# Optimization experiments

Measured on AMD Instinct MI355X. Metric: run time of the kernel, lower is better.

## Reference

```python
import jax, jax.numpy as jnp
import numpy as np

T, B = 100, 512
DIMS = [700, 512, 20]
ALPHA = 0.8   # 1 - dt/tau_s = 1 - 0.001/0.005
BETA = 0.9    # 1 - dt/tau_m = 1 - 0.001/0.010
THR = 1.0     # snntorch default threshold


@jax.custom_vjp
def spike(x):
    # Heaviside with ATan surrogate gradient (snntorch default, alpha=2)
    return (x > 0).astype(x.dtype)

def _spike_fwd(x):
    return spike(x), x

def _spike_bwd(x, g):
    # d/dx atan surrogate with alpha=2: 1 / (1 + (pi*x)^2)
    return (g / (1.0 + (jnp.pi * x) ** 2),)

spike.defvjp(_spike_fwd, _spike_bwd)


def setup_inputs() -> dict:
    key = jax.random.key(0)
    kx, k1, k2 = jax.random.split(key, 3)
    x = jax.random.uniform(kx, (T, B, DIMS[0]), dtype=jnp.float32)
    # kaiming_normal_ on weight [d2, d1]: std = sqrt(2 / fan_in), fan_in = d1
    W1 = jax.random.normal(k1, (DIMS[1], DIMS[0]), dtype=jnp.float32) * np.sqrt(2.0 / DIMS[0])
    W2 = jax.random.normal(k2, (DIMS[2], DIMS[1]), dtype=jnp.float32) * np.sqrt(2.0 / DIMS[1])
    return {"x": x, "W1": W1, "W2": W2}


def _spiking_linear(x, W):
    # x: [T, B, d_in], W: [d_out, d_in]
    pre = jnp.einsum('tbi,oi->tbo', x, W)  # per-timestep F.linear, batched over T

    def step(carry, p):
        syn, mem = carry
        syn = ALPHA * syn + p
        # reset from previous-step membrane, detached (snntorch mem_reset)
        reset = jax.lax.stop_gradient((mem > THR).astype(p.dtype))
        mem = (BETA * mem + syn) * (1.0 - reset)  # reset_mechanism='zero'
        spk = spike(mem - THR)
        return (syn, mem), spk

    z = jnp.zeros(pre.shape[1:], dtype=pre.dtype)
    _, spks = jax.lax.scan(step, (z, z), pre)
    return spks  # [T, B, d_out]


def reference(x, W1, W2):
    x = x.astype(jnp.float32)
    s1 = _spiking_linear(x, W1)
    s2 = _spiking_linear(s1, W2)
    # SNN2.forward returns (out, all_spikes=[layer1_spikes, layer2_spikes])
    return (s2, s1, s2)
```

## Files before the change

kernel.cpp:

```cpp
#include <hip/hip_runtime.h>

#define T_STEPS 100
#define BATCH   512
#define D0      700
#define D1      512
#define D2      20
#define M_ROWS  (T_STEPS * BATCH)

#define OFF_S2A 0
#define OFF_S1  (T_STEPS * BATCH * D2)
#define OFF_S2B (OFF_S1 + T_STEPS * BATCH * D1)

__device__ __constant__ const float kALPHA = 0.8f;
__device__ __constant__ const float kBETA  = 0.9f;
__device__ __constant__ const float kTHR   = 1.0f;

constexpr int BM = 128, BN = 128, BK = 32;

__device__ __forceinline__ int swz(int k, int m) {
    const int c = m >> 2;
    const int cpos = c ^ ((c >> 3) & 3) ^ ((k >> 2) & 7);
    return k * BM + (cpos << 2) + (m & 3);
}

__global__ __launch_bounds__(256)
void gemm1_kernel(const float* __restrict__ A, const float* __restrict__ W,
                  float* __restrict__ C) {
    __shared__ float As[BK * BM];
    __shared__ float Ws[BK * BN];

    const int tid  = threadIdx.x;
    const int row0 = blockIdx.x * BM;
    const int col0 = blockIdx.y * BN;

    const int tx = tid & 15;
    const int ty = tid >> 4;

    const int ca0 = (2 * ty)     ^ (((2 * ty)     >> 3) & 3);
    const int ca1 = (2 * ty + 1) ^ (((2 * ty + 1) >> 3) & 3);
    const int cb0 = (2 * tx)     ^ (((2 * tx)     >> 3) & 3);
    const int cb1 = (2 * tx + 1) ^ (((2 * tx + 1) >> 3) & 3);

    float acc[8][8];
#pragma unroll
    for (int i = 0; i < 8; ++i)
#pragma unroll
        for (int j = 0; j < 8; ++j) acc[i][j] = 0.f;

    const int NT = (D0 + BK - 1) / BK;
    for (int kt = 0; kt < NT; ++kt) {
        const int k0 = kt * BK;
#pragma unroll
        for (int l = 0; l < 4; ++l) {
            const int f  = tid + l * 256;
            const int r  = f >> 3;
            const int c4 = f & 7;
            const int k  = c4 * 4;
            const int gk = k0 + k;

            float4 v, w;
            if (gk + 3 < D0) {
                v = *(const float4*)(A + (size_t)(row0 + r) * D0 + gk);
                w = *(const float4*)(W + (size_t)(col0 + r) * D0 + gk);
            } else {
                const float* ap = A + (size_t)(row0 + r) * D0;
                const float* wp = W + (size_t)(col0 + r) * D0;
                v.x = (gk + 0 < D0) ? ap[gk + 0] : 0.f;
                v.y = (gk + 1 < D0) ? ap[gk + 1] : 0.f;
                v.z = (gk + 2 < D0) ? ap[gk + 2] : 0.f;
                v.w = (gk + 3 < D0) ? ap[gk + 3] : 0.f;
                w.x = (gk + 0 < D0) ? wp[gk + 0] : 0.f;
                w.y = (gk + 1 < D0) ? wp[gk + 1] : 0.f;
                w.z = (gk + 2 < D0) ? wp[gk + 2] : 0.f;
                w.w = (gk + 3 < D0) ? wp[gk + 3] : 0.f;
            }
            As[swz(k + 0, r)] = v.x; As[swz(k + 1, r)] = v.y;
            As[swz(k + 2, r)] = v.z; As[swz(k + 3, r)] = v.w;
            Ws[swz(k + 0, r)] = w.x; Ws[swz(k + 1, r)] = w.y;
            Ws[swz(k + 2, r)] = w.z; Ws[swz(k + 3, r)] = w.w;
        }
        __syncthreads();

#pragma unroll
        for (int k = 0; k < BK; ++k) {
            const int kx = (k >> 2) & 7;
            const int kb = k * BM;
            float a[8], b[8];
            *(float4*)&a[0] = *(const float4*)&As[kb + ((ca0 ^ kx) << 2)];
            *(float4*)&a[4] = *(const float4*)&As[kb + ((ca1 ^ kx) << 2)];
            *(float4*)&b[0] = *(const float4*)&Ws[kb + ((cb0 ^ kx) << 2)];
            *(float4*)&b[4] = *(const float4*)&Ws[kb + ((cb1 ^ kx) << 2)];
#pragma unroll
            for (int i = 0; i < 8; ++i)
#pragma unroll
                for (int j = 0; j < 8; ++j)
                    acc[i][j] = fmaf(a[i], b[j], acc[i][j]);
        }
        __syncthreads();
    }

#pragma unroll
    for (int i = 0; i < 8; ++i) {
        float* cp = C + (size_t)(row0 + ty * 8 + i) * D1 + col0 + tx * 8;
        float4 v0 = make_float4(acc[i][0], acc[i][1], acc[i][2], acc[i][3]);
        float4 v1 = make_float4(acc[i][4], acc[i][5], acc[i][6], acc[i][7]);
        *(float4*)(cp + 0) = v0;
        *(float4*)(cp + 4) = v1;
    }
}

__global__ __launch_bounds__(256)
void scan1_kernel(float* __restrict__ buf) {
#pragma clang fp contract(off)
    const int idx = blockIdx.x * blockDim.x + threadIdx.x;
    const int stride = BATCH * D1;
    float syn = 0.f, mem = 0.f;
    float* p = buf + idx;
    for (int t = 0; t < T_STEPS; ++t) {
        const float pre = p[(size_t)t * stride];
        float a = kALPHA * syn;
        syn = a + pre;
        const float reset = (mem > kTHR) ? 1.f : 0.f;
        float bm = kBETA * mem;
        mem = (bm + syn) * (1.f - reset);
        p[(size_t)t * stride] = (mem > kTHR) ? 1.f : 0.f;
    }
}

__global__ __launch_bounds__(256)
void gemm2_kernel(const float* __restrict__ S1, const float* __restrict__ W2,
                  float* __restrict__ C) {
    __shared__ float Wsh[D2 * D1];
    for (int i = threadIdx.x; i < (D2 * D1) / 4; i += 256)
        ((float4*)Wsh)[i] = ((const float4*)W2)[i];
    __syncthreads();

    const int r  = threadIdx.x >> 2;
    const int kq = threadIdx.x & 3;
    const int m  = blockIdx.x * 64 + r;

    const float4* src = (const float4*)(S1 + (size_t)m * D1 + kq * 128);
    float acc[D2];
#pragma unroll
    for (int o = 0; o < D2; ++o) acc[o] = 0.f;

    for (int j = 0; j < 32; ++j) {
        const float4 v = src[j];
        const float* wbase = Wsh + kq * 128 + j * 4;
#pragma unroll
        for (int o = 0; o < D2; ++o) {
            const float4 w = *(const float4*)(wbase + o * D1);
            acc[o] += v.x * w.x + v.y * w.y + v.z * w.z + v.w * w.w;
        }
    }
#pragma unroll
    for (int o = 0; o < D2; ++o) {
        acc[o] += __shfl_xor(acc[o], 1);
        acc[o] += __shfl_xor(acc[o], 2);
    }
    if (kq == 0) {
        float* cp = C + (size_t)m * D2;
#pragma unroll
        for (int o = 0; o < D2; o += 4)
            *(float4*)(cp + o) = make_float4(acc[o], acc[o + 1], acc[o + 2], acc[o + 3]);
    }
}

__global__ __launch_bounds__(256)
void scan2_kernel(float* __restrict__ buf, float* __restrict__ dup) {
#pragma clang fp contract(off)
    const int idx = blockIdx.x * blockDim.x + threadIdx.x;
    const int stride = BATCH * D2;
    float syn = 0.f, mem = 0.f;
    for (int t = 0; t < T_STEPS; ++t) {
        const size_t off = (size_t)t * stride + idx;
        const float pre = buf[off];
        float a = kALPHA * syn;
        syn = a + pre;
        const float reset = (mem > kTHR) ? 1.f : 0.f;
        float bm = kBETA * mem;
        mem = (bm + syn) * (1.f - reset);
        const float s = (mem > kTHR) ? 1.f : 0.f;
        buf[off] = s;
        dup[off] = s;
    }
}

extern "C" void kernel_launch(void* const* d_in, const int* in_sizes, int n_in,
                              void* d_out, int out_size, void* d_ws, size_t ws_size,
                              hipStream_t stream) {
    const float* x  = (const float*)d_in[0];
    const float* W1 = (const float*)d_in[1];
    const float* W2 = (const float*)d_in[2];
    float* out = (float*)d_out;

    float* s2a = out + OFF_S2A;
    float* s1  = out + OFF_S1;
    float* s2b = out + OFF_S2B;

    dim3 g1(M_ROWS / BM, D1 / BN);
    gemm1_kernel<<<g1, 256, 0, stream>>>(x, W1, s1);

    scan1_kernel<<<(BATCH * D1) / 256, 256, 0, stream>>>(s1);

    gemm2_kernel<<<M_ROWS / 64, 256, 0, stream>>>(s1, W2, s2a);

    scan2_kernel<<<(BATCH * D2) / 256, 256, 0, stream>>>(s2a, s2b);
}
```

Baseline: 605.1 us.

## Double-buffer shared memory tiles in gemm1 with register prefetch

Restructures the first GEMM's K loop to keep two shared-memory tile buffers. Global loads for the next K tile go into registers before the current tile's FMA work, then are stored into the alternate buffer, leaving one barrier per iteration instead of two. This is meant to hide global memory latency behind compute. It doubles LDS use to 32 KB per block and holds 8 float4 prefetch registers per thread, which may lower occupancy.

Result: slower. 741.8 us (+22.6%).

```diff
diff --git a/kernel.cpp b/kernel.cpp
--- a/kernel.cpp
+++ b/kernel.cpp
@@ -16,6 +16,7 @@
 __device__ __constant__ const float kTHR   = 1.0f;
 
 constexpr int BM = 128, BN = 128, BK = 32;
+constexpr int TILE_F = BK * BM;
 
 __device__ __forceinline__ int swz(int k, int m) {
     const int c = m >> 2;
@@ -26,8 +27,8 @@
 __global__ __launch_bounds__(256)
 void gemm1_kernel(const float* __restrict__ A, const float* __restrict__ W,
                   float* __restrict__ C) {
-    __shared__ float As[BK * BM];
-    __shared__ float Ws[BK * BN];
+    __shared__ float As[2 * TILE_F];
+    __shared__ float Ws[2 * TILE_F];
 
     const int tid  = threadIdx.x;
     const int row0 = blockIdx.x * BM;
@@ -47,57 +48,84 @@
 #pragma unroll
         for (int j = 0; j < 8; ++j) acc[i][j] = 0.f;
 
+    float4 va[4], vw[4];
+
     const int NT = (D0 + BK - 1) / BK;
-    for (int kt = 0; kt < NT; ++kt) {
+
+    auto LOAD = [&](int kt) {
         const int k0 = kt * BK;
 #pragma unroll
         for (int l = 0; l < 4; ++l) {
             const int f  = tid + l * 256;
             const int r  = f >> 3;
-            const int c4 = f & 7;
-            const int k  = c4 * 4;
+            const int k  = (f & 7) * 4;
             const int gk = k0 + k;
-
-            float4 v, w;
             if (gk + 3 < D0) {
-                v = *(const float4*)(A + (size_t)(row0 + r) * D0 + gk);
-                w = *(const float4*)(W + (size_t)(col0 + r) * D0 + gk);
+                va[l] = *(const float4*)(A + (size_t)(row0 + r) * D0 + gk);
+                vw[l] = *(const float4*)(W + (size_t)(col0 + r) * D0 + gk);
             } else {
                 const float* ap = A + (size_t)(row0 + r) * D0;
                 const float* wp = W + (size_t)(col0 + r) * D0;
-                v.x = (gk + 0 < D0) ? ap[gk + 0] : 0.f;
-                v.y = (gk + 1 < D0) ? ap[gk + 1] : 0.f;
-                v.z = (gk + 2 < D0) ? ap[gk + 2] : 0.f;
-                v.w = (gk + 3 < D0) ? ap[gk + 3] : 0.f;
-                w.x = (gk + 0 < D0) ? wp[gk + 0] : 0.f;
-                w.y = (gk + 1 < D0) ? wp[gk + 1] : 0.f;
-                w.z = (gk + 2 < D0) ? wp[gk + 2] : 0.f;
-                w.w = (gk + 3 < D0) ? wp[gk + 3] : 0.f;
+                va[l].x = (gk + 0 < D0) ? ap[gk + 0] : 0.f;
+                va[l].y = (gk + 1 < D0) ? ap[gk + 1] : 0.f;
+                va[l].z = (gk + 2 < D0) ? ap[gk + 2] : 0.f;
+                va[l].w = (gk + 3 < D0) ? ap[gk + 3] : 0.f;
+                vw[l].x = (gk + 0 < D0) ? wp[gk + 0] : 0.f;
+                vw[l].y = (gk + 1 < D0) ? wp[gk + 1] : 0.f;
+                vw[l].z = (gk + 2 < D0) ? wp[gk + 2] : 0.f;
+                vw[l].w = (gk + 3 < D0) ? wp[gk + 3] : 0.f;
             }
-            As[swz(k + 0, r)] = v.x; As[swz(k + 1, r)] = v.y;
-            As[swz(k + 2, r)] = v.z; As[swz(k + 3, r)] = v.w;
-            Ws[swz(k + 0, r)] = w.x; Ws[swz(k + 1, r)] = w.y;
-            Ws[swz(k + 2, r)] = w.z; Ws[swz(k + 3, r)] = w.w;
-        }
-        __syncthreads();
-
+        }
+    };
+
+    auto STORE = [&](int buf) {
+        float* as = As + buf * TILE_F;
+        float* ws = Ws + buf * TILE_F;
+#pragma unroll
+        for (int l = 0; l < 4; ++l) {
+            const int f = tid + l * 256;
+            const int r = f >> 3;
+            const int k = (f & 7) * 4;
+            as[swz(k + 0, r)] = va[l].x; as[swz(k + 1, r)] = va[l].y;
+            as[swz(k + 2, r)] = va[l].z; as[swz(k + 3, r)] = va[l].w;
+            ws[swz(k + 0, r)] = vw[l].x; ws[swz(k + 1, r)] = vw[l].y;
+            ws[swz(k + 2, r)] = vw[l].z; ws[swz(k + 3, r)] = vw[l].w;
+        }
+    };
+
+    auto COMPUTE = [&](int buf) {
+        const float* as = As + buf * TILE_F;
+        const float* ws = Ws + buf * TILE_F;
 #pragma unroll
         for (int k = 0; k < BK; ++k) {
             const int kx = (k >> 2) & 7;
             const int kb = k * BM;
             float a[8], b[8];
-            *(float4*)&a[0] = *(const float4*)&As[kb + ((ca0 ^ kx) << 2)];
-            *(float4*)&a[4] = *(const float4*)&As[kb + ((ca1 ^ kx) << 2)];
-            *(float4*)&b[0] = *(const float4*)&Ws[kb + ((cb0 ^ kx) << 2)];
-            *(float4*)&b[4] = *(const float4*)&Ws[kb + ((cb1 ^ kx) << 2)];
+            *(float4*)&a[0] = *(const float4*)&as[kb + ((ca0 ^ kx) << 2)];
+            *(float4*)&a[4] = *(const float4*)&as[kb + ((ca1 ^ kx) << 2)];
+            *(float4*)&b[0] = *(const float4*)&ws[kb + ((cb0 ^ kx) << 2)];
+            *(float4*)&b[4] = *(const float4*)&ws[kb + ((cb1 ^ kx) << 2)];
 #pragma unroll
             for (int i = 0; i < 8; ++i)
 #pragma unroll
                 for (int j = 0; j < 8; ++j)
                     acc[i][j] = fmaf(a[i], b[j], acc[i][j]);
         }
+    };
+
+    LOAD(0);
+    STORE(0);
+    __syncthreads();
+
+    int cur = 0;
+    for (int kt = 0; kt < NT - 1; ++kt) {
+        LOAD(kt + 1);
+        COMPUTE(cur);
+        STORE(cur ^ 1);
         __syncthreads();
-    }
+        cur ^= 1;
+    }
+    COMPUTE(cur);
 
 #pragma unroll
     for (int i = 0; i < 8; ++i) {
```
